# Optimization experiments

Measured on AMD Instinct MI355X. Metric: run time of the kernel, lower is better.

The kernel has to match this reference:

```python
import jax, jax.numpy as jnp
import numpy as np

B, S, T = 64, 48, 48
E, H = 512, 1024
V_SRC, V_TGT = 32000, 32000
PAD = 0


def setup_inputs() -> dict:
    key = jax.random.key(0)
    ks = jax.random.split(key, 24)
    def g(k, shape, scale=0.05):
        return jax.random.normal(k, shape, dtype=jnp.float32) * scale
    return {
        "src_ids": jax.random.randint(ks[0], (S, B), 0, V_SRC),
        "tgt_ids": jax.random.randint(ks[1], (T, B), 0, V_TGT),
        "src_lengths": S,
        "src_emb": g(ks[2], (V_SRC, E)).at[PAD].set(0.0),
        "tgt_emb": g(ks[3], (V_TGT, E)).at[PAD].set(0.0),
        "cnn_w": g(ks[4], (E, E, 2)),
        "cnn_b": g(ks[5], (E,)),
        "enc_Wih_f": g(ks[6], (4 * H, E)),
        "enc_Whh_f": g(ks[7], (4 * H, H)),
        "enc_bih_f": g(ks[8], (4 * H,)),
        "enc_bhh_f": g(ks[9], (4 * H,)),
        "enc_Wih_b": g(ks[10], (4 * H, E)),
        "enc_Whh_b": g(ks[11], (4 * H, H)),
        "enc_bih_b": g(ks[12], (4 * H,)),
        "enc_bhh_b": g(ks[13], (4 * H,)),
        "dec_Wih": g(ks[14], (4 * H, E + H)),
        "dec_Whh": g(ks[15], (4 * H, H)),
        "dec_bih": g(ks[16], (4 * H,)),
        "dec_bhh": g(ks[17], (4 * H,)),
        "Wh": g(ks[18], (H, 2 * H)),
        "Wc": g(ks[19], (H, 2 * H)),
        "Watt": g(ks[20], (H, 2 * H)),
        "Wcomb": g(ks[21], (H, 3 * H)),
        "Wvocab": g(ks[22], (V_TGT, H)),
    }


def _lstm_cell(x, h, c, Wih, Whh, bih, bhh):
    gates = x @ Wih.T + h @ Whh.T + bih + bhh  # (b, 4h)
    i, f, g, o = jnp.split(gates, 4, axis=-1)
    c_new = jax.nn.sigmoid(f) * c + jax.nn.sigmoid(i) * jnp.tanh(g)
    h_new = jax.nn.sigmoid(o) * jnp.tanh(c_new)
    return h_new, c_new


def _forward(src_ids, tgt_ids,
             src_emb, tgt_emb, cnn_w, cnn_b,
             enc_Wih_f, enc_Whh_f, enc_bih_f, enc_bhh_f,
             enc_Wih_b, enc_Whh_b, enc_bih_b, enc_bhh_b,
             dec_Wih, dec_Whh, dec_bih, dec_bhh,
             Wh, Wc, Watt, Wcomb, Wvocab):
    b = src_ids.shape[1]
    h = Wh.shape[0]
    # ---- encode ----
    X = src_emb[src_ids]                       # (S, b, E)
    Xc = jnp.transpose(X, (1, 2, 0))           # (b, E, S)
    # Conv1d kernel_size=2, padding='same' in torch pads (left=0, right=1)
    Xc = jax.lax.conv_general_dilated(Xc, cnn_w, window_strides=(1,),
                                      padding=[(0, 1)],
                                      dimension_numbers=("NCH", "OIH", "NCH"))
    Xc = Xc + cnn_b[None, :, None]
    X = jnp.transpose(Xc, (2, 0, 1))           # (S, b, E)

    h0 = jnp.zeros((b, h), dtype=X.dtype)
    def fstep(carry, x_t):
        hh, cc = carry
        hh, cc = _lstm_cell(x_t, hh, cc, enc_Wih_f, enc_Whh_f, enc_bih_f, enc_bhh_f)
        return (hh, cc), hh
    def bstep(carry, x_t):
        hh, cc = carry
        hh, cc = _lstm_cell(x_t, hh, cc, enc_Wih_b, enc_Whh_b, enc_bih_b, enc_bhh_b)
        return (hh, cc), hh
    (hf, cf), out_f = jax.lax.scan(fstep, (h0, h0), X)
    (hb, cb), out_b = jax.lax.scan(bstep, (h0, h0), X[::-1])
    out_b = out_b[::-1]
    enc_hiddens = jnp.concatenate([out_f, out_b], axis=-1)   # (S, b, 2h)
    enc_hiddens = jnp.transpose(enc_hiddens, (1, 0, 2))      # (b, S, 2h)
    dec_h = jnp.concatenate([hf, hb], axis=1) @ Wh.T         # (b, h)
    dec_c = jnp.concatenate([cf, cb], axis=1) @ Wc.T         # (b, h)

    # ---- decode ----
    enc_proj = enc_hiddens @ Watt.T            # (b, S, h)
    enc_mask = jnp.zeros((b, enc_hiddens.shape[1]), dtype=bool)  # all full length
    Y = tgt_emb[tgt_ids[:-1]]                  # (T-1, b, E)

    def dstep(carry, Y_t):
        hh, cc, o_prev = carry
        ybar = jnp.concatenate([o_prev, Y_t], axis=1)        # (b, h+E)
        hh, cc = _lstm_cell(ybar, hh, cc, dec_Wih, dec_Whh, dec_bih, dec_bhh)
        e_t = jnp.einsum("bh,bsh->bs", hh, enc_proj)
        e_t = jnp.where(enc_mask, -jnp.inf, e_t)
        alpha = jax.nn.softmax(e_t, axis=-1)
        a_t = jnp.einsum("bs,bsd->bd", alpha, enc_hiddens)   # (b, 2h)
        O_t = jnp.tanh(jnp.concatenate([a_t, hh], axis=1) @ Wcomb.T)  # dropout rate 0
        return (hh, cc, O_t), O_t

    o0 = jnp.zeros((b, h), dtype=X.dtype)
    _, combined = jax.lax.scan(dstep, (dec_h, dec_c, o0), Y)  # (T-1, b, h)

    P = jax.nn.log_softmax(combined @ Wvocab.T, axis=-1)      # (T-1, b, V)
    gold = tgt_ids[1:]                                        # (T-1, b)
    logp = jnp.take_along_axis(P, gold[..., None], axis=-1)[..., 0]
    tmask = (gold != PAD).astype(P.dtype)
    return (logp * tmask).sum(axis=0)                         # (b,)


def reference(src_ids, tgt_ids, src_lengths,
              src_emb, tgt_emb, cnn_w, cnn_b,
              enc_Wih_f, enc_Whh_f, enc_bih_f, enc_bhh_f,
              enc_Wih_b, enc_Whh_b, enc_bih_b, enc_bhh_b,
              dec_Wih, dec_Whh, dec_bih, dec_bhh,
              Wh, Wc, Watt, Wcomb, Wvocab):
    # src_lengths == S for every sentence (packed seq degenerates to full-length LSTM)
    return _forward(src_ids, tgt_ids, src_emb, tgt_emb, cnn_w, cnn_b,
                    enc_Wih_f, enc_Whh_f, enc_bih_f, enc_bhh_f,
                    enc_Wih_b, enc_Whh_b, enc_bih_b, enc_bhh_b,
                    dec_Wih, dec_Whh, dec_bih, dec_bhh,
                    Wh, Wc, Watt, Wcomb, Wvocab)
```

## Files before the change

kernel.cpp:

```cpp
#include <hip/hip_runtime.h>
#include <hip/hip_bf16.h>
#include <math.h>

using f32x4 = __attribute__((ext_vector_type(4))) float;
using s16x8 = __attribute__((ext_vector_type(8))) short;
typedef unsigned short u16;
typedef unsigned int u32;
typedef unsigned long long u64;

#define MFMA16(a,b,c) __builtin_amdgcn_mfma_f32_16x16x32_bf16(a,b,c,0,0,0)
#define SCOPE_A __HIP_MEMORY_SCOPE_AGENT
#define FP 16

__device__ __forceinline__ float bf2f(u16 u){
  union { u32 i; float f; } v; v.i = ((u32)u) << 16; return v.f;
}
__device__ __forceinline__ u16 f2bf(float f){
  union { float f; u32 i; } v; v.f = f;
  u32 x = v.i;
  return (u16)((x + 0x7fffu + ((x >> 16) & 1u)) >> 16);
}
__device__ __forceinline__ float sigm(float x){ return 1.0f/(1.0f + expf(-x)); }

__device__ __forceinline__ s16x8 pack8(const float* p){
  s16x8 r;
  #pragma unroll
  for (int i = 0; i < 8; ++i) r[i] = (short)f2bf(p[i]);
  return r;
}

__device__ __forceinline__ s16x8 coh_ld16B(const u16* p){
  union { u64 q[2]; s16x8 v; } u;
  u.q[0] = __hip_atomic_load((const u64*)p,       __ATOMIC_RELAXED, SCOPE_A);
  u.q[1] = __hip_atomic_load((const u64*)(p + 4), __ATOMIC_RELAXED, SCOPE_A);
  return u.v;
}
__device__ __forceinline__ u32 coh_ld32(const void* p){
  return __hip_atomic_load((const u32*)p, __ATOMIC_RELAXED, SCOPE_A);
}
__device__ __forceinline__ void coh_st32(void* p, u32 v){
  __hip_atomic_store((u32*)p, v, __ATOMIC_RELAXED, SCOPE_A);
}
__device__ __forceinline__ float u2f(u32 u){ union { u32 i; float f; } v; v.i = u; return v.f; }
__device__ __forceinline__ u32 f2u(float f){ union { float f; u32 i; } v; v.f = f; return v.i; }

__device__ __forceinline__ void poll(const int* flags, int n, int gen){
  for (int i = threadIdx.x; i < n; i += 256)
    while (__hip_atomic_load(flags + i*FP, __ATOMIC_RELAXED, SCOPE_A) < gen)
      __builtin_amdgcn_s_sleep(1);
  __syncthreads();
}
__device__ __forceinline__ void setflag(int* flag, int gen){
  __syncthreads();
  if (threadIdx.x == 0)
    __hip_atomic_store(flag, gen, __ATOMIC_RELAXED, SCOPE_A);
}

__device__ __forceinline__ void gemm_k1024_coh(
    const u16* ap, const char* wb0, const char* wb1, int xo, int addb,
    f32x4& a0, f32x4& a1)
{
  #pragma unroll
  for (int c = 0; c < 2; ++c){
    s16x8 st[16];
    #pragma unroll
    for (int q = 0; q < 16; ++q) st[q] = coh_ld16B(ap + c*512 + q*32);
    #pragma unroll
    for (int q = 0; q < 16; ++q){
      int cb = (addb + (c*512 + q*32)*2) ^ xo;
      a0 = MFMA16(st[q], *(const s16x8*)(wb0 + cb), a0);
      a1 = MFMA16(st[q], *(const s16x8*)(wb1 + cb), a1);
    }
  }
}

__global__ void k_zero(float* __restrict__ p, long n){
  long i = (long)blockIdx.x*blockDim.x + threadIdx.x;
  long st = (long)gridDim.x*blockDim.x;
  for (; i < n; i += st) p[i] = 0.0f;
}

__global__ void k_cast_bf16(const float* __restrict__ src, u16* __restrict__ dst, long n){
  long i = ((long)blockIdx.x*blockDim.x + threadIdx.x)*4;
  long st = (long)gridDim.x*blockDim.x*4;
  for (; i < n; i += st){
    float4 v = *(const float4*)(src + i);
    *(ushort4*)(dst + i) = make_ushort4(f2bf(v.x), f2bf(v.y), f2bf(v.z), f2bf(v.w));
  }
}

__global__ void k_addv(const float* __restrict__ a, const float* __restrict__ b,
                       float* __restrict__ d, int n){
  int i = blockIdx.x*blockDim.x + threadIdx.x;
  if (i < n) d[i] = a[i] + b[i];
}

__global__ void k_repack_conv(const float* __restrict__ w, u16* __restrict__ dst){
  int i = blockIdx.x*256 + threadIdx.x;
  int o = i >> 9, ii = i & 511;
  dst[(size_t)o*1024 + ii]       = f2bf(w[((size_t)o*512 + ii)*2 + 0]);
  dst[(size_t)o*1024 + 512 + ii] = f2bf(w[((size_t)o*512 + ii)*2 + 1]);
}

__global__ void k_build_wy(const float* __restrict__ dWih, u16* __restrict__ Wy){
  int i = blockIdx.x*256 + threadIdx.x;
  int r = i >> 9, c = i & 511;
  Wy[(size_t)r*512 + c] = f2bf(dWih[(size_t)r*1536 + 1024 + c]);
}

__global__ void k_split_wcomb(const float* __restrict__ Wcomb,
                              u16* __restrict__ Wca, u16* __restrict__ Whp){
  int r = blockIdx.x;
  for (int c = threadIdx.x; c < 2048; c += 256)
    Wca[(size_t)r*2048 + c] = f2bf(Wcomb[(size_t)r*3072 + c]);
  for (int c = threadIdx.x; c < 1024; c += 256)
    Whp[(size_t)r*1024 + c] = f2bf(Wcomb[(size_t)r*3072 + 2048 + c]);
}

__global__ void k_gather_src(const int* __restrict__ ids, const float* __restrict__ emb,
                             u16* __restrict__ Aconv){
  int s = blockIdx.x;
  int b = blockIdx.y;
  int e = threadIdx.x*4;
  float4 v = make_float4(0.f,0.f,0.f,0.f);
  if (s < 48){ int id = ids[s*64 + b]; v = *(const float4*)(emb + (size_t)id*512 + e); }
  ushort4 u = make_ushort4(f2bf(v.x), f2bf(v.y), f2bf(v.z), f2bf(v.w));
  if (s < 48) *(ushort4*)(Aconv + ((size_t)(s*64 + b))*1024 + e) = u;
  if (s >= 1) *(ushort4*)(Aconv + ((size_t)((s-1)*64 + b))*1024 + 512 + e) = u;
}

__global__ void k_gather_y(const int* __restrict__ ids, const float* __restrict__ emb,
                           u16* __restrict__ Y){
  int t = blockIdx.x; int b = blockIdx.y; int e = threadIdx.x*4;
  int id = ids[t*64 + b];
  float4 v = *(const float4*)(emb + (size_t)id*512 + e);
  *(ushort4*)(Y + ((size_t)(t*64 + b))*512 + e) = make_ushort4(f2bf(v.x), f2bf(v.y), f2bf(v.z), f2bf(v.w));
}

template<bool OUT_BF16>
__global__ __launch_bounds__(256) void k_gemm(
    const u16* __restrict__ A0, long lda0,
    const u16* __restrict__ A1, long lda1, int ksplit,
    const u16* __restrict__ W, int K,
    void* __restrict__ Out, long ldc,
    const float* __restrict__ bias)
{
  __shared__ __align__(16) u16 As[64][72];
  __shared__ __align__(16) u16 Ws[64][72];
  const int t = threadIdx.x;
  const int m0 = blockIdx.x*64, n0 = blockIdx.y*64;
  const int w = t >> 6, l = t & 63, lr = l & 15, lh = l >> 4;
  const int sr = t >> 2, sk = (t & 3) << 4;

  f32x4 acc[4] = {{0,0,0,0},{0,0,0,0},{0,0,0,0},{0,0,0,0}};

  for (int kc = 0; kc < K; kc += 64){
    {
      const u16* wp = W + (size_t)(n0 + sr)*K + kc + sk;
      *(s16x8*)&Ws[sr][sk]     = *(const s16x8*)wp;
      *(s16x8*)&Ws[sr][sk + 8] = *(const s16x8*)(wp + 8);
    }
    {
      const u16* ap = (kc < ksplit)
        ? A0 + (size_t)(m0 + sr)*lda0 + kc
        : A1 + (size_t)(m0 + sr)*lda1 + (kc - ksplit);
      ap += sk;
      *(s16x8*)&As[sr][sk]     = *(const s16x8*)ap;
      *(s16x8*)&As[sr][sk + 8] = *(const s16x8*)(ap + 8);
    }
    __syncthreads();
    #pragma unroll
    for (int kk = 0; kk < 64; kk += 32){
      s16x8 a = *(const s16x8*)&As[w*16 + lr][kk + lh*8];
      #pragma unroll
      for (int ct = 0; ct < 4; ++ct){
        s16x8 bfr = *(const s16x8*)&Ws[ct*16 + lr][kk + lh*8];
        acc[ct] = MFMA16(a, bfr, acc[ct]);
      }
    }
    __syncthreads();
  }
  #pragma unroll
  for (int ct = 0; ct < 4; ++ct){
    #pragma unroll
    for (int rr = 0; rr < 4; ++rr){
      long row = m0 + w*16 + lh*4 + rr;
      long col = n0 + ct*16 + lr;
      float v = acc[ct][rr];
      if (bias) v += bias[col];
      long oi = row*ldc + col;
      if (OUT_BF16) ((u16*)Out)[oi] = f2bf(v);
      else          ((float*)Out)[oi] = v;
    }
  }
}

__global__ __launch_bounds__(256) void k_enc_persist(
    const float* __restrict__ WhhF, const float* __restrict__ WhhB,
    const u16* __restrict__ Gf, const u16* __restrict__ Gb,
    u16* __restrict__ hF0, u16* __restrict__ hF1,
    u16* __restrict__ hB0, u16* __restrict__ hB1,
    float* __restrict__ cF, float* __restrict__ cB,
    u16* __restrict__ Aatt, u16* __restrict__ cfbf, u16* __restrict__ cbbf,
    int* Eflags)
{
  extern __shared__ char smem[];
  const int t = threadIdx.x, blk = blockIdx.x;
  const int dir = blk >> 6;
  const int j0 = (blk & 63) << 4;
  const float* Wsrc = dir ? WhhB : WhhF;
  const u16* G = dir ? Gb : Gf;
  float* c = dir ? cB : cF;
  u16* cobf = dir ? cbbf : cfbf;
  u16* h0 = dir ? hB0 : hF0;
  u16* h1 = dir ? hB1 : hF1;

  for (int q = t; q < 64*128; q += 256){
    int row = q >> 7;
    int ck = (q & 127) << 3;
    int wrow = ((row >> 4)*1024) + j0 + (row & 15);
    s16x8 pk = pack8(Wsrc + (size_t)wrow*1024 + ck);
    *(s16x8*)(smem + row*2048 + ((ck*2) ^ ((row & 7) << 4))) = pk;
  }
  __syncthreads();

  const int w = t >> 6, l = t & 63, lr = l & 15, lh = l >> 4;
  const int lane_m = w*16 + lr;
  const int koff = lh*8;
  const char* wp0 = smem + lr*2048;
  const char* wp1 = smem + (16 + lr)*2048;
  const char* wp2 = smem + (32 + lr)*2048;
  const char* wp3 = smem + (48 + lr)*2048;
  const int xo = (lr & 7) << 4;
  const int j = j0 + lr;
  int* myflags = Eflags + dir*64*FP;
  const int myidx = blk & 63;

  for (int s = 0; s < 48; ++s){
    const u16* hin = (s & 1) ? h1 : h0;
    u16* hout      = (s & 1) ? h0 : h1;
    const int time = dir ? 47 - s : s;
    if (s) poll(myflags, 64, s);
    f32x4 a0 = {0,0,0,0}, a1 = {0,0,0,0}, a2 = {0,0,0,0}, a3 = {0,0,0,0};
    const u16* ap = hin + (size_t)lane_m*1024 + koff;
    #pragma unroll
    for (int cc = 0; cc < 2; ++cc){
      s16x8 st[16];
      #pragma unroll
      for (int q = 0; q < 16; ++q) st[q] = coh_ld16B(ap + cc*512 + q*32);
      #pragma unroll
      for (int q = 0; q < 16; ++q){
        int cb = ((cc*512 + q*32 + koff)*2) ^ xo;
        a0 = MFMA16(st[q], *(const s16x8*)(wp0 + cb), a0);
        a1 = MFMA16(st[q], *(const s16x8*)(wp1 + cb), a1);
        a2 = MFMA16(st[q], *(const s16x8*)(wp2 + cb), a2);
        a3 = MFMA16(st[q], *(const s16x8*)(wp3 + cb), a3);
      }
    }
    #pragma unroll
    for (int rr = 0; rr < 4; ++rr){
      int b = w*16 + lh*4 + rr;
      size_t grow = ((size_t)time*64 + b)*4096;
      float gi = a0[rr] + bf2f(G[grow + j]);
      float gf = a1[rr] + bf2f(G[grow + 1024 + j]);
      float gg = a2[rr] + bf2f(G[grow + 2048 + j]);
      float go = a3[rr] + bf2f(G[grow + 3072 + j]);
      float cn = sigm(gf)*c[b*1024 + j] + sigm(gi)*tanhf(gg);
      float hn = sigm(go)*tanhf(cn);
      c[b*1024 + j] = cn;
      u16 hb = f2bf(hn);
      u32 hi2 = __shfl_down((u32)hb, 1);
      if ((lr & 1) == 0)
        coh_st32((u32*)hout + ((b*1024 + j) >> 1), (u32)hb | (hi2 << 16));
      Aatt[((size_t)b*48 + time)*2048 + dir*1024 + j] = hb;
      if (s == 47) cobf[b*1024 + j] = f2bf(cn);
    }
    setflag(myflags + myidx*FP, s + 1);
  }
}

__global__ __launch_bounds__(256) void k_dec_persist(
    const float* __restrict__ dWih, const float* __restrict__ dWhh,
    const u16* __restrict__ Gy,
    const u16* __restrict__ encP, const u16* __restrict__ encWc,
    const u16* __restrict__ Whp,
    u16* __restrict__ hbf0, u16* __restrict__ hbf1,
    float* __restrict__ cdec,
    float* __restrict__ hpart, u16* __restrict__ Cbf,
    const u16* __restrict__ obf_zero,
    int* Gflags, int* G2flags, int* Cflags)
{
  extern __shared__ char smem[];
  const int t = threadIdx.x, blk = blockIdx.x;
  const int w = t >> 6, l = t & 63, lr = l & 15, lh = l >> 4;
  const int lane_m = w*16 + lr;
  const int koff = lh*8;
  const int xo = (lr & 7) << 4;

  if (blk < 128){
    const int j0 = blk << 3;
    for (int q = t; q < 32*256; q += 256){
      int row = q >> 8;
      int ck = (q & 255) << 3;
      int wrow = ((row >> 3)*1024) + j0 + (row & 7);
      const float* src = (ck < 1024) ? dWih + (size_t)wrow*1536 + ck
                                     : dWhh + (size_t)wrow*1024 + (ck - 1024);
      s16x8 pk = pack8(src);
      *(s16x8*)(smem + row*4096 + ((ck*2) ^ ((row & 7) << 4))) = pk;
    }
    char* WhpL = smem + 131072;
    for (int q = t; q < 8*128; q += 256){
      int row = q >> 7, ck = (q & 127) << 3;
      s16x8 v = *(const s16x8*)(Whp + (size_t)(j0 + row)*1024 + ck);
      *(s16x8*)(WhpL + row*2048 + ((ck*2) ^ ((row & 7) << 4))) = v;
    }
    __syncthreads();
    const char* wp0 = smem + lr*4096;
    const char* wp1 = smem + (16 + lr)*4096;
    const char* wph = WhpL + (lr & 7)*2048;
    const int jj = lr & 7, gsel = lr >> 3;
    const int j = j0 + jj;

    s16x8 hreg[32];
    {
      const u16* ap = hbf0 + (size_t)lane_m*1024 + koff;
      #pragma unroll
      for (int q = 0; q < 32; ++q) hreg[q] = coh_ld16B(ap + q*32);
    }

    for (int tt = 0; tt < 47; ++tt){
      u16* hout = (tt & 1) ? hbf0 : hbf1;
      f32x4 a0 = {0,0,0,0}, a1 = {0,0,0,0};
      #pragma unroll
      for (int q = 0; q < 32; ++q){
        int cb = ((1024 + q*32 + koff)*2) ^ xo;
        a0 = MFMA16(hreg[q], *(const s16x8*)(wp0 + cb), a0);
        a1 = MFMA16(hreg[q], *(const s16x8*)(wp1 + cb), a1);
      }
      if (tt) poll(Cflags, 64, tt);
      const u16* Ao = tt ? (Cbf + (size_t)(tt - 1)*65536) : obf_zero;
      gemm_k1024_coh(Ao + (size_t)lane_m*1024 + koff, wp0, wp1, xo, koff*2, a0, a1);
      #pragma unroll
      for (int rr = 0; rr < 4; ++rr){
        float v0 = a0[rr], v1 = a1[rr];
        float p0 = __shfl_xor(v0, 8, 64);
        float p1 = __shfl_xor(v1, 8, 64);
        if (gsel == 0){
          int b = w*16 + lh*4 + rr;
          size_t grow = ((size_t)tt*64 + b)*4096;
          float gi = v0 + bf2f(Gy[grow + j]);
          float gf = p0 + bf2f(Gy[grow + 1024 + j]);
          float gg = v1 + bf2f(Gy[grow + 2048 + j]);
          float go = p1 + bf2f(Gy[grow + 3072 + j]);
          float cn = sigm(gf)*cdec[b*1024 + j] + sigm(gi)*tanhf(gg);
          float hn = sigm(go)*tanhf(cn);
          cdec[b*1024 + j] = cn;
          u16 hb = f2bf(hn);
          u32 hi2 = __shfl_down((u32)hb, 1);
          if ((jj & 1) == 0)
            coh_st32((u32*)hout + ((b*1024 + j) >> 1), (u32)hb | (hi2 << 16));
        }
      }
      setflag(Gflags + blk*FP, tt + 1);
      poll(Gflags, 128, tt + 1);
      {
        const u16* ap = hout + (size_t)lane_m*1024 + koff;
        #pragma unroll
        for (int q = 0; q < 32; ++q) hreg[q] = coh_ld16B(ap + q*32);
      }
      f32x4 hp = {0,0,0,0};
      #pragma unroll
      for (int q = 0; q < 32; ++q){
        int cb = ((q*32 + koff)*2) ^ xo;
        s16x8 bw = {0,0,0,0,0,0,0,0};
        if (lr < 8) bw = *(const s16x8*)(wph + cb);
        hp = MFMA16(hreg[q], bw, hp);
      }
      if (lr < 8){
        #pragma unroll
        for (int rr = 0; rr < 4; ++rr)
          coh_st32(&hpart[(size_t)(w*16 + lh*4 + rr)*1024 + j0 + lr], f2u(hp[rr]));
      }
      setflag(G2flags + blk*FP, tt + 1);
    }
  } else {
    const int b = blk - 128;
    u16* encPL = (u16*)smem;
    float* hs  = (float*)(smem + 98304);
    float* es  = (float*)(smem + 102400);
    float* al  = es + 48;
    float* sred= al + 48;
    for (int q = t; q < 48*128; q += 256){
      int row = q >> 7, ck = (q & 127) << 3;
      *(s16x8*)&encPL[row*1024 + ck] =
        *(const s16x8*)(encP + ((size_t)b*48 + row)*1024 + ck);
    }
    __syncthreads();

    for (int tt = 0; tt < 47; ++tt){
      poll(Gflags, 128, tt + 1);
      const u16* hpost = (tt & 1) ? hbf0 : hbf1;
      const u32* h32 = (const u32*)hpost + b*512;
      for (int i = t; i < 512; i += 256){
        u32 v = coh_ld32(h32 + i);
        hs[2*i]     = bf2f((u16)(v & 0xffff));
        hs[2*i + 1] = bf2f((u16)(v >> 16));
      }
      __syncthreads();
      for (int s2 = w; s2 < 48; s2 += 4){
        float p = 0.f;
        #pragma unroll
        for (int i = 0; i < 16; ++i)
          p += hs[l + 64*i]*bf2f(encPL[s2*1024 + l + 64*i]);
        #pragma unroll
        for (int d = 32; d >= 1; d >>= 1) p += __shfl_xor(p, d, 64);
        if (l == 0) es[s2] = p;
      }
      __syncthreads();
      if (t == 0){
        float m = es[0];
        for (int s2 = 1; s2 < 48; ++s2) m = fmaxf(m, es[s2]);
        float su = 0.f;
        for (int s2 = 0; s2 < 48; ++s2) su += expf(es[s2] - m);
        sred[0] = m; sred[1] = 1.0f/su;
      }
      __syncthreads();
      if (t < 48) al[t] = expf(es[t] - sred[0])*sred[1];
      __syncthreads();
      poll(G2flags, 128, tt + 1);
      int c0 = t*4;
      float4 hpv;
      {
        union { u64 q[2]; float4 v; } u;
        const u64* hp64 = (const u64*)(hpart + (size_t)b*1024 + c0);
        u.q[0] = __hip_atomic_load(hp64,     __ATOMIC_RELAXED, SCOPE_A);
        u.q[1] = __hip_atomic_load(hp64 + 1, __ATOMIC_RELAXED, SCOPE_A);
        hpv = u.v;
      }
      float acc0 = 0.f, acc1 = 0.f, acc2 = 0.f, acc3 = 0.f;
      const u16* ew = encWc + (size_t)b*48*1024 + c0;
      #pragma unroll 4
      for (int s2 = 0; s2 < 48; ++s2){
        float wgt = al[s2];
        ushort4 e4 = *(const ushort4*)(ew + (size_t)s2*1024);
        acc0 += wgt*bf2f(e4.x); acc1 += wgt*bf2f(e4.y);
        acc2 += wgt*bf2f(e4.z); acc3 += wgt*bf2f(e4.w);
      }
      float v0 = tanhf(hpv.x + acc0), v1 = tanhf(hpv.y + acc1);
      float v2 = tanhf(hpv.z + acc2), v3 = tanhf(hpv.w + acc3);
      size_t oi = (size_t)tt*65536 + (size_t)b*1024 + c0;
      coh_st32((u32*)Cbf + (oi >> 1),     (u32)f2bf(v0) | ((u32)f2bf(v1) << 16));
      coh_st32((u32*)Cbf + (oi >> 1) + 1, (u32)f2bf(v2) | ((u32)f2bf(v3) << 16));
      setflag(Cflags + b*FP, tt + 1);
    }
  }
}

#define VNS 25
__global__ __launch_bounds__(256) void k_vocab_lse(
    const u16* __restrict__ Cbf, const u16* __restrict__ Wv, float2* __restrict__ partials)
{
  __shared__ __align__(16) u16 As[128][72];
  __shared__ __align__(16) u16 Bs[128][72];
  __shared__ float2 mg[128][2];
  int rb = blockIdx.x, sp = blockIdx.y;
  int m0 = rb*128;
  int t = threadIdx.x, w = t >> 6, l = t & 63, lr = l & 15, lh = l >> 4;
  int wr = w >> 1, wc = w & 1;
  int sr = t >> 1, sk = (t & 1) << 5;

  float mrun[4][4], srun[4][4];
  #pragma unroll
  for (int m = 0; m < 4; ++m)
    #pragma unroll
    for (int rr = 0; rr < 4; ++rr){ mrun[m][rr] = -INFINITY; srun[m][rr] = 0.f; }

  for (int nt = 0; nt < 10; ++nt){
    int n0 = sp*1280 + nt*128;
    f32x4 acc[4][4];
    #pragma unroll
    for (int m = 0; m < 4; ++m)
      #pragma unroll
      for (int n = 0; n < 4; ++n) acc[m][n] = (f32x4){0,0,0,0};

    for (int kc = 0; kc < 1024; kc += 64){
      int ar = m0 + sr; if (ar > 3007) ar = 3007;
      const u16* ap = Cbf + (size_t)ar*1024 + kc + sk;
      const u16* wp = Wv + (size_t)(n0 + sr)*1024 + kc + sk;
      #pragma unroll
      for (int q = 0; q < 4; ++q){
        *(s16x8*)&As[sr][sk + q*8] = *(const s16x8*)(ap + q*8);
        *(s16x8*)&Bs[sr][sk + q*8] = *(const s16x8*)(wp + q*8);
      }
      __syncthreads();
      #pragma unroll
      for (int kk = 0; kk < 64; kk += 32){
        s16x8 af[4], bf[4];
        #pragma unroll
        for (int m = 0; m < 4; ++m)
          af[m] = *(const s16x8*)&As[wr*64 + m*16 + lr][kk + lh*8];
        #pragma unroll
        for (int n = 0; n < 4; ++n)
          bf[n] = *(const s16x8*)&Bs[wc*64 + n*16 + lr][kk + lh*8];
        #pragma unroll
        for (int m = 0; m < 4; ++m)
          #pragma unroll
          for (int n = 0; n < 4; ++n)
            acc[m][n] = MFMA16(af[m], bf[n], acc[m][n]);
      }
      __syncthreads();
    }
    #pragma unroll
    for (int m = 0; m < 4; ++m){
      #pragma unroll
      for (int rr = 0; rr < 4; ++rr){
        float tm = fmaxf(fmaxf(acc[m][0][rr], acc[m][1][rr]),
                         fmaxf(acc[m][2][rr], acc[m][3][rr]));
        #pragma unroll
        for (int d = 1; d < 16; d <<= 1) tm = fmaxf(tm, __shfl_xor(tm, d, 64));
        float ts = expf(acc[m][0][rr] - tm) + expf(acc[m][1][rr] - tm)
                 + expf(acc[m][2][rr] - tm) + expf(acc[m][3][rr] - tm);
        #pragma unroll
        for (int d = 1; d < 16; d <<= 1) ts += __shfl_xor(ts, d, 64);
        if (tm > mrun[m][rr]){ srun[m][rr] = srun[m][rr]*expf(mrun[m][rr] - tm) + ts; mrun[m][rr] = tm; }
        else srun[m][rr] += ts*expf(tm - mrun[m][rr]);
      }
    }
  }
  __syncthreads();
  if (lr == 0){
    #pragma unroll
    for (int m = 0; m < 4; ++m)
      #pragma unroll
      for (int rr = 0; rr < 4; ++rr)
        mg[wr*64 + m*16 + lh*4 + rr][wc] = make_float2(mrun[m][rr], srun[m][rr]);
  }
  __syncthreads();
  if (t < 128){
    float2 p0 = mg[t][0], p1 = mg[t][1];
    float m = fmaxf(p0.x, p1.x);
    float s = p0.y*expf(p0.x - m) + p1.y*expf(p1.x - m);
    long row = m0 + t;
    if (row < 3008) partials[row*VNS + sp] = make_float2(m, s);
  }
}

__global__ void k_lse(const float2* __restrict__ partials, float* __restrict__ lse){
  int r = blockIdx.x*256 + threadIdx.x;
  if (r >= 3008) return;
  float m = -INFINITY, s = 0.f;
  for (int i = 0; i < VNS; ++i){
    float2 p = partials[r*VNS + i];
    if (p.x > m){ s = s*expf(m - p.x) + p.y; m = p.x; }
    else s += p.y*expf(p.x - m);
  }
  lse[r] = m + logf(s);
}

__global__ __launch_bounds__(256) void k_gold(const u16* __restrict__ Cbf,
                                              const u16* __restrict__ Wv,
                                              const int* __restrict__ tgt,
                                              float* __restrict__ gold){
  int w = threadIdx.x >> 6, l = threadIdx.x & 63;
  int r = blockIdx.x*4 + w;
  int tt = r >> 6, b = r & 63;
  int gid = tgt[(tt + 1)*64 + b];
  const u16* cp = Cbf + (size_t)r*1024;
  const u16* wp = Wv + (size_t)gid*1024;
  float p = 0.f;
  for (int i = l; i < 1024; i += 64) p += bf2f(cp[i])*bf2f(wp[i]);
  for (int d = 32; d >= 1; d >>= 1) p += __shfl_xor(p, d, 64);
  if (l == 0) gold[r] = p;
}

__global__ void k_final(const float* __restrict__ gold, const float* __restrict__ lse,
                        const int* __restrict__ tgt, float* __restrict__ out){
  int b = threadIdx.x;
  if (b >= 64) return;
  float acc = 0.f;
  for (int t = 0; t < 47; ++t){
    int gid = tgt[(t + 1)*64 + b];
    if (gid != 0) acc += gold[t*64 + b] - lse[t*64 + b];
  }
  out[b] = acc;
}

extern "C" void kernel_launch(void* const* d_in, const int* in_sizes, int n_in,
                              void* d_out, int out_size, void* d_ws, size_t ws_size,
                              hipStream_t stream)
{
  (void)in_sizes; (void)n_in; (void)out_size; (void)ws_size;
  const int*   src_ids = (const int*)d_in[0];
  const int*   tgt_ids = (const int*)d_in[1];
  const float* src_emb = (const float*)d_in[3];
  const float* tgt_emb = (const float*)d_in[4];
  const float* cnn_w   = (const float*)d_in[5];
  const float* cnn_b   = (const float*)d_in[6];
  const float* eWih_f  = (const float*)d_in[7];
  const float* eWhh_f  = (const float*)d_in[8];
  const float* ebih_f  = (const float*)d_in[9];
  const float* ebhh_f  = (const float*)d_in[10];
  const float* eWih_b  = (const float*)d_in[11];
  const float* eWhh_b  = (const float*)d_in[12];
  const float* ebih_b  = (const float*)d_in[13];
  const float* ebhh_b  = (const float*)d_in[14];
  const float* dWih    = (const float*)d_in[15];
  const float* dWhh    = (const float*)d_in[16];
  const float* dbih    = (const float*)d_in[17];
  const float* dbhh    = (const float*)d_in[18];
  const float* Wh      = (const float*)d_in[19];
  const float* Wc      = (const float*)d_in[20];
  const float* Watt    = (const float*)d_in[21];
  const float* Wcomb   = (const float*)d_in[22];
  const float* Wvocab  = (const float*)d_in[23];

  char* ws = (char*)d_ws;
  size_t off = 0;
  auto alloc = [&](size_t bytes)->char*{
    char* p = ws + off;
    off = (off + bytes + 255) & ~(size_t)255;
    return p;
  };

  u16* hF0      = (u16*)alloc((size_t)65536*2);
  u16* hB0      = (u16*)alloc((size_t)65536*2);
  float* cF     = (float*)alloc((size_t)65536*4);
  float* cB     = (float*)alloc((size_t)65536*4);
  u16* obf_zero = (u16*)alloc((size_t)65536*2);
  int* bar      = (int*)alloc(40960);
  size_t zero_floats = ((size_t)131072*3 + (size_t)262144*2 + 40960)/4;
  int* Eflags  = bar;
  int* Gflags  = bar + 2048;
  int* G2flags = bar + 4096;
  int* Cflags  = bar + 6144;

  u16* hF1      = (u16*)alloc((size_t)65536*2);
  u16* hB1      = (u16*)alloc((size_t)65536*2);

  u16* Wconv_bf = (u16*)alloc((size_t)512*1024*2);
  u16* Wih_f_bf = (u16*)alloc((size_t)4096*512*2);
  u16* Wih_b_bf = (u16*)alloc((size_t)4096*512*2);
  u16* Wy_bf    = (u16*)alloc((size_t)4096*512*2);
  u16* Wh_bf    = (u16*)alloc((size_t)1024*2048*2);
  u16* Wc_bf    = (u16*)alloc((size_t)1024*2048*2);
  u16* Watt_bf  = (u16*)alloc((size_t)1024*2048*2);
  u16* Wca_bf   = (u16*)alloc((size_t)1024*2048*2);
  u16* Whp_bf   = (u16*)alloc((size_t)1024*1024*2);
  u16* Wv_bf    = (u16*)alloc((size_t)32000*1024*2);
  float* benc_f = (float*)alloc(4096*4);
  float* benc_b = (float*)alloc(4096*4);
  float* bdec   = (float*)alloc(4096*4);

  u16* Aconv    = (u16*)alloc((size_t)3072*1024*2);
  u16* Xc       = (u16*)alloc((size_t)3072*512*2);
  u16* Gf       = (u16*)alloc((size_t)3072*4096*2);
  u16* Gb       = (u16*)alloc((size_t)3072*4096*2);
  u16* Ybf      = (u16*)alloc((size_t)3008*512*2);
  u16* Gy       = (u16*)alloc((size_t)3008*4096*2);
  u16* Aatt     = (u16*)alloc((size_t)3072*2048*2);
  u16* encP     = (u16*)alloc((size_t)3072*1024*2);
  u16* encWc    = (u16*)alloc((size_t)3072*1024*2);
  u16* cfbf     = (u16*)alloc((size_t)65536*2);
  u16* cbbf     = (u16*)alloc((size_t)65536*2);
  u16* hbf0     = (u16*)alloc((size_t)65536*2);
  u16* hbf1     = (u16*)alloc((size_t)65536*2);
  float* cdec   = (float*)alloc((size_t)65536*4);
  float* hpartD = (float*)alloc((size_t)65536*4);
  u16* Cbf      = (u16*)alloc((size_t)3008*1024*2);
  float2* partials=(float2*)alloc((size_t)3008*VNS*8);
  float* lse    = (float*)alloc(3008*4);
  float* gold   = (float*)alloc(3008*4);

  k_zero<<<256, 256, 0, stream>>>((float*)hF0, (long)zero_floats);

  auto cgrid = [](long n)->int{ long g = (n/4 + 255)/256; return (int)(g > 1024 ? 1024 : g); };
  k_cast_bf16<<<cgrid(4096*512), 256, 0, stream>>>(eWih_f, Wih_f_bf, (long)4096*512);
  k_cast_bf16<<<cgrid(4096*512), 256, 0, stream>>>(eWih_b, Wih_b_bf, (long)4096*512);
  k_cast_bf16<<<cgrid(1024*2048), 256, 0, stream>>>(Wh, Wh_bf, (long)1024*2048);
  k_cast_bf16<<<cgrid(1024*2048), 256, 0, stream>>>(Wc, Wc_bf, (long)1024*2048);
  k_cast_bf16<<<cgrid(1024*2048), 256, 0, stream>>>(Watt, Watt_bf, (long)1024*2048);
  k_cast_bf16<<<cgrid((long)32000*1024), 256, 0, stream>>>(Wvocab, Wv_bf, (long)32000*1024);

  k_addv<<<16, 256, 0, stream>>>(ebih_f, ebhh_f, benc_f, 4096);
  k_addv<<<16, 256, 0, stream>>>(ebih_b, ebhh_b, benc_b, 4096);
  k_addv<<<16, 256, 0, stream>>>(dbih, dbhh, bdec, 4096);

  k_repack_conv<<<1024, 256, 0, stream>>>(cnn_w, Wconv_bf);
  k_build_wy<<<8192, 256, 0, stream>>>(dWih, Wy_bf);
  k_split_wcomb<<<1024, 256, 0, stream>>>(Wcomb, Wca_bf, Whp_bf);

  k_gather_src<<<dim3(49, 64), 128, 0, stream>>>(src_ids, src_emb, Aconv);
  k_gather_y<<<dim3(47, 64), 128, 0, stream>>>(tgt_ids, tgt_emb, Ybf);

  k_gemm<true><<<dim3(48, 8), 256, 0, stream>>>(
      Aconv, 1024, Aconv, 1024, 1024, Wconv_bf, 1024, Xc, 512, cnn_b);
  k_gemm<true><<<dim3(48, 64), 256, 0, stream>>>(
      Xc, 512, Xc, 512, 512, Wih_f_bf, 512, Gf, 4096, benc_f);
  k_gemm<true><<<dim3(48, 64), 256, 0, stream>>>(
      Xc, 512, Xc, 512, 512, Wih_b_bf, 512, Gb, 4096, benc_b);
  k_gemm<true><<<dim3(47, 64), 256, 0, stream>>>(
      Ybf, 512, Ybf, 512, 512, Wy_bf, 512, Gy, 4096, bdec);

  k_enc_persist<<<128, 256, 131072, stream>>>(
      eWhh_f, eWhh_b, Gf, Gb, hF0, hF1, hB0, hB1, cF, cB,
      Aatt, cfbf, cbbf, Eflags);

  k_gemm<true><<<dim3(1, 16), 256, 0, stream>>>(
      hF0, 1024, hB0, 1024, 1024, Wh_bf, 2048, hbf0, 1024, nullptr);
  k_gemm<false><<<dim3(1, 16), 256, 0, stream>>>(
      cfbf, 1024, cbbf, 1024, 1024, Wc_bf, 2048, cdec, 1024, nullptr);
  k_gemm<true><<<dim3(48, 16), 256, 0, stream>>>(
      Aatt, 2048, Aatt, 2048, 2048, Watt_bf, 2048, encP, 1024, nullptr);
  k_gemm<true><<<dim3(48, 16), 256, 0, stream>>>(
      Aatt, 2048, Aatt, 2048, 2048, Wca_bf, 2048, encWc, 1024, nullptr);

  k_dec_persist<<<192, 256, 147456, stream>>>(
      dWih, dWhh, Gy, encP, encWc, Whp_bf, hbf0, hbf1, cdec,
      hpartD, Cbf, obf_zero, Gflags, G2flags, Cflags);

  k_vocab_lse<<<dim3(24, VNS), 256, 0, stream>>>(Cbf, Wv_bf, partials);
  k_lse<<<12, 256, 0, stream>>>(partials, lse);
  k_gold<<<752, 256, 0, stream>>>(Cbf, Wv_bf, tgt_ids, gold);
  k_final<<<1, 64, 0, stream>>>(gold, lse, tgt_ids, (float*)d_out);
}
```

Before: 2.769 ms.

## Use per-step hidden buffers with plain loads and repack gate precompute layout

Replaces the ping-pong hidden-state buffers in the encoder and decoder persistent kernels with one buffer per timestep. Because no address is ever rewritten, the agent-scope atomic loads can become plain vector loads without stale-cache hazards. The input-gate GEMMs now write a packed [time][j][gate][batch] layout, so each lane's four gate reads are close together instead of 1024 elements apart. This costs more memory and leaves cross-block visibility depending on never-before-touched addresses and relaxed flag ordering, which is a correctness risk.

Result: faster. 2.585 ms (-6.6%).

```diff
diff --git a/kernel.cpp b/kernel.cpp
--- a/kernel.cpp
+++ b/kernel.cpp
@@ -29,15 +29,6 @@
   return r;
 }
 
-__device__ __forceinline__ s16x8 coh_ld16B(const u16* p){
-  union { u64 q[2]; s16x8 v; } u;
-  u.q[0] = __hip_atomic_load((const u64*)p,       __ATOMIC_RELAXED, SCOPE_A);
-  u.q[1] = __hip_atomic_load((const u64*)(p + 4), __ATOMIC_RELAXED, SCOPE_A);
-  return u.v;
-}
-__device__ __forceinline__ u32 coh_ld32(const void* p){
-  return __hip_atomic_load((const u32*)p, __ATOMIC_RELAXED, SCOPE_A);
-}
 __device__ __forceinline__ void coh_st32(void* p, u32 v){
   __hip_atomic_store((u32*)p, v, __ATOMIC_RELAXED, SCOPE_A);
 }
@@ -56,7 +47,7 @@
     __hip_atomic_store(flag, gen, __ATOMIC_RELAXED, SCOPE_A);
 }
 
-__device__ __forceinline__ void gemm_k1024_coh(
+__device__ __forceinline__ void gemm_k1024(
     const u16* ap, const char* wb0, const char* wb1, int xo, int addb,
     f32x4& a0, f32x4& a1)
 {
@@ -64,7 +55,7 @@
   for (int c = 0; c < 2; ++c){
     s16x8 st[16];
     #pragma unroll
-    for (int q = 0; q < 16; ++q) st[q] = coh_ld16B(ap + c*512 + q*32);
+    for (int q = 0; q < 16; ++q) st[q] = *(const s16x8*)(ap + c*512 + q*32);
     #pragma unroll
     for (int q = 0; q < 16; ++q){
       int cb = (addb + (c*512 + q*32)*2) ^ xo;
@@ -137,7 +128,7 @@
   *(ushort4*)(Y + ((size_t)(t*64 + b))*512 + e) = make_ushort4(f2bf(v.x), f2bf(v.y), f2bf(v.z), f2bf(v.w));
 }
 
-template<bool OUT_BF16>
+template<bool OUT_BF16, bool PACKG>
 __global__ __launch_bounds__(256) void k_gemm(
     const u16* __restrict__ A0, long lda0,
     const u16* __restrict__ A1, long lda1, int ksplit,
@@ -188,18 +179,23 @@
       long col = n0 + ct*16 + lr;
       float v = acc[ct][rr];
       if (bias) v += bias[col];
-      long oi = row*ldc + col;
-      if (OUT_BF16) ((u16*)Out)[oi] = f2bf(v);
-      else          ((float*)Out)[oi] = v;
+      if (PACKG){
+        long time = row >> 6, b = row & 63, g = col >> 10, j = col & 1023;
+        ((u16*)Out)[((time*1024 + j)*4 + g)*64 + b] = f2bf(v);
+      } else {
+        long oi = row*ldc + col;
+        if (OUT_BF16) ((u16*)Out)[oi] = f2bf(v);
+        else          ((float*)Out)[oi] = v;
+      }
     }
   }
 }
 
 __global__ __launch_bounds__(256) void k_enc_persist(
     const float* __restrict__ WhhF, const float* __restrict__ WhhB,
-    const u16* __restrict__ Gf, const u16* __restrict__ Gb,
-    u16* __restrict__ hF0, u16* __restrict__ hF1,
-    u16* __restrict__ hB0, u16* __restrict__ hB1,
+    const u16* __restrict__ GfP, const u16* __restrict__ GbP,
+    u16* __restrict__ hEF, u16* __restrict__ hEB,
+    const u16* __restrict__ hzero,
     float* __restrict__ cF, float* __restrict__ cB,
     u16* __restrict__ Aatt, u16* __restrict__ cfbf, u16* __restrict__ cbbf,
     int* Eflags)
@@ -209,11 +205,10 @@
   const int dir = blk >> 6;
   const int j0 = (blk & 63) << 4;
   const float* Wsrc = dir ? WhhB : WhhF;
-  const u16* G = dir ? Gb : Gf;
+  const u16* GP = dir ? GbP : GfP;
   float* c = dir ? cB : cF;
   u16* cobf = dir ? cbbf : cfbf;
-  u16* h0 = dir ? hB0 : hF0;
-  u16* h1 = dir ? hB1 : hF1;
+  u16* hE = dir ? hEB : hEF;
 
   for (int q = t; q < 64*128; q += 256){
     int row = q >> 7;
@@ -237,8 +232,8 @@
   const int myidx = blk & 63;
 
   for (int s = 0; s < 48; ++s){
-    const u16* hin = (s & 1) ? h1 : h0;
-    u16* hout      = (s & 1) ? h0 : h1;
+    const u16* hin = s ? (hE + (size_t)(s - 1)*65536) : hzero;
+    u16* hout      = hE + (size_t)s*65536;
     const int time = dir ? 47 - s : s;
     if (s) poll(myflags, 64, s);
     f32x4 a0 = {0,0,0,0}, a1 = {0,0,0,0}, a2 = {0,0,0,0}, a3 = {0,0,0,0};
@@ -247,7 +242,7 @@
     for (int cc = 0; cc < 2; ++cc){
       s16x8 st[16];
       #pragma unroll
-      for (int q = 0; q < 16; ++q) st[q] = coh_ld16B(ap + cc*512 + q*32);
+      for (int q = 0; q < 16; ++q) st[q] = *(const s16x8*)(ap + cc*512 + q*32);
       #pragma unroll
       for (int q = 0; q < 16; ++q){
         int cb = ((cc*512 + q*32 + koff)*2) ^ xo;
@@ -260,11 +255,11 @@
     #pragma unroll
     for (int rr = 0; rr < 4; ++rr){
       int b = w*16 + lh*4 + rr;
-      size_t grow = ((size_t)time*64 + b)*4096;
-      float gi = a0[rr] + bf2f(G[grow + j]);
-      float gf = a1[rr] + bf2f(G[grow + 1024 + j]);
-      float gg = a2[rr] + bf2f(G[grow + 2048 + j]);
-      float go = a3[rr] + bf2f(G[grow + 3072 + j]);
+      const u16* gp = GP + (((size_t)time*1024 + j)*4)*64 + b;
+      float gi = a0[rr] + bf2f(gp[0]);
+      float gf = a1[rr] + bf2f(gp[64]);
+      float gg = a2[rr] + bf2f(gp[128]);
+      float go = a3[rr] + bf2f(gp[192]);
       float cn = sigm(gf)*c[b*1024 + j] + sigm(gi)*tanhf(gg);
       float hn = sigm(go)*tanhf(cn);
       c[b*1024 + j] = cn;
@@ -281,12 +276,12 @@
 
 __global__ __launch_bounds__(256) void k_dec_persist(
     const float* __restrict__ dWih, const float* __restrict__ dWhh,
-    const u16* __restrict__ Gy,
+    const u16* __restrict__ GyP,
     const u16* __restrict__ encP, const u16* __restrict__ encWc,
     const u16* __restrict__ Whp,
-    u16* __restrict__ hbf0, u16* __restrict__ hbf1,
+    const u16* __restrict__ hbinit, u16* __restrict__ hD,
     float* __restrict__ cdec,
-    float* __restrict__ hpart, u16* __restrict__ Cbf,
+    float* __restrict__ hp, u16* __restrict__ Cbf,
     const u16* __restrict__ obf_zero,
     int* Gflags, int* G2flags, int* Cflags)
 {
@@ -323,13 +318,13 @@
 
     s16x8 hreg[32];
     {
-      const u16* ap = hbf0 + (size_t)lane_m*1024 + koff;
-      #pragma unroll
-      for (int q = 0; q < 32; ++q) hreg[q] = coh_ld16B(ap + q*32);
+      const u16* ap = hbinit + (size_t)lane_m*1024 + koff;
+      #pragma unroll
+      for (int q = 0; q < 32; ++q) hreg[q] = *(const s16x8*)(ap + q*32);
     }
 
     for (int tt = 0; tt < 47; ++tt){
-      u16* hout = (tt & 1) ? hbf0 : hbf1;
+      u16* hout = hD + (size_t)tt*65536;
       f32x4 a0 = {0,0,0,0}, a1 = {0,0,0,0};
       #pragma unroll
       for (int q = 0; q < 32; ++q){
@@ -339,7 +334,7 @@
       }
       if (tt) poll(Cflags, 64, tt);
       const u16* Ao = tt ? (Cbf + (size_t)(tt - 1)*65536) : obf_zero;
-      gemm_k1024_coh(Ao + (size_t)lane_m*1024 + koff, wp0, wp1, xo, koff*2, a0, a1);
+      gemm_k1024(Ao + (size_t)lane_m*1024 + koff, wp0, wp1, xo, koff*2, a0, a1);
       #pragma unroll
       for (int rr = 0; rr < 4; ++rr){
         float v0 = a0[rr], v1 = a1[rr];
@@ -347,11 +342,11 @@
         float p1 = __shfl_xor(v1, 8, 64);
         if (gsel == 0){
           int b = w*16 + lh*4 + rr;
-          size_t grow = ((size_t)tt*64 + b)*4096;
-          float gi = v0 + bf2f(Gy[grow + j]);
-          float gf = p0 + bf2f(Gy[grow + 1024 + j]);
-          float gg = v1 + bf2f(Gy[grow + 2048 + j]);
-          float go = p1 + bf2f(Gy[grow + 3072 + j]);
+          const u16* gp = GyP + (((size_t)tt*1024 + j)*4)*64 + b;
+          float gi = v0 + bf2f(gp[0]);
+          float gf = p0 + bf2f(gp[64]);
+          float gg = v1 + bf2f(gp[128]);
+          float go = p1 + bf2f(gp[192]);
           float cn = sigm(gf)*cdec[b*1024 + j] + sigm(gi)*tanhf(gg);
           float hn = sigm(go)*tanhf(cn);
           cdec[b*1024 + j] = cn;
@@ -366,20 +361,21 @@
       {
         const u16* ap = hout + (size_t)lane_m*1024 + koff;
         #pragma unroll
-        for (int q = 0; q < 32; ++q) hreg[q] = coh_ld16B(ap + q*32);
-      }
-      f32x4 hp = {0,0,0,0};
+        for (int q = 0; q < 32; ++q) hreg[q] = *(const s16x8*)(ap + q*32);
+      }
+      f32x4 hpacc = {0,0,0,0};
       #pragma unroll
       for (int q = 0; q < 32; ++q){
         int cb = ((q*32 + koff)*2) ^ xo;
         s16x8 bw = {0,0,0,0,0,0,0,0};
         if (lr < 8) bw = *(const s16x8*)(wph + cb);
-        hp = MFMA16(hreg[q], bw, hp);
+        hpacc = MFMA16(hreg[q], bw, hpacc);
       }
       if (lr < 8){
+        float* hpout = hp + (size_t)tt*65536;
         #pragma unroll
         for (int rr = 0; rr < 4; ++rr)
-          coh_st32(&hpart[(size_t)(w*16 + lh*4 + rr)*1024 + j0 + lr], f2u(hp[rr]));
+          coh_st32(&hpout[(size_t)(w*16 + lh*4 + rr)*1024 + j0 + lr], f2u(hpacc[rr]));
       }
       setflag(G2flags + blk*FP, tt + 1);
     }
@@ -399,12 +395,13 @@
 
     for (int tt = 0; tt < 47; ++tt){
       poll(Gflags, 128, tt + 1);
-      const u16* hpost = (tt & 1) ? hbf0 : hbf1;
-      const u32* h32 = (const u32*)hpost + b*512;
-      for (int i = t; i < 512; i += 256){
-        u32 v = coh_ld32(h32 + i);
-        hs[2*i]     = bf2f((u16)(v & 0xffff));
-        hs[2*i + 1] = bf2f((u16)(v >> 16));
+      const u16* hrow = hD + (size_t)tt*65536 + (size_t)b*1024;
+      {
+        ushort4 v4 = ((const ushort4*)hrow)[t];
+        hs[4*t]     = bf2f(v4.x);
+        hs[4*t + 1] = bf2f(v4.y);
+        hs[4*t + 2] = bf2f(v4.z);
+        hs[4*t + 3] = bf2f(v4.w);
       }
       __syncthreads();
       for (int s2 = w; s2 < 48; s2 += 4){
@@ -429,14 +426,7 @@
       __syncthreads();
       poll(G2flags, 128, tt + 1);
       int c0 = t*4;
-      float4 hpv;
-      {
-        union { u64 q[2]; float4 v; } u;
-        const u64* hp64 = (const u64*)(hpart + (size_t)b*1024 + c0);
-        u.q[0] = __hip_atomic_load(hp64,     __ATOMIC_RELAXED, SCOPE_A);
-        u.q[1] = __hip_atomic_load(hp64 + 1, __ATOMIC_RELAXED, SCOPE_A);
-        hpv = u.v;
-      }
+      float4 hpv = *(const float4*)(hp + (size_t)tt*65536 + (size_t)b*1024 + c0);
       float acc0 = 0.f, acc1 = 0.f, acc2 = 0.f, acc3 = 0.f;
       const u16* ew = encWc + (size_t)b*48*1024 + c0;
       #pragma unroll 4
@@ -622,20 +612,15 @@
     return p;
   };
 
-  u16* hF0      = (u16*)alloc((size_t)65536*2);
-  u16* hB0      = (u16*)alloc((size_t)65536*2);
   float* cF     = (float*)alloc((size_t)65536*4);
   float* cB     = (float*)alloc((size_t)65536*4);
   u16* obf_zero = (u16*)alloc((size_t)65536*2);
   int* bar      = (int*)alloc(40960);
-  size_t zero_floats = ((size_t)131072*3 + (size_t)262144*2 + 40960)/4;
+  size_t zero_floats = ((size_t)262144*2 + 131072 + 40960)/4;
   int* Eflags  = bar;
   int* Gflags  = bar + 2048;
   int* G2flags = bar + 4096;
   int* Cflags  = bar + 6144;
-
-  u16* hF1      = (u16*)alloc((size_t)65536*2);
-  u16* hB1      = (u16*)alloc((size_t)65536*2);
 
   u16* Wconv_bf = (u16*)alloc((size_t)512*1024*2);
   u16* Wih_f_bf = (u16*)alloc((size_t)4096*512*2);
@@ -653,25 +638,27 @@
 
   u16* Aconv    = (u16*)alloc((size_t)3072*1024*2);
   u16* Xc       = (u16*)alloc((size_t)3072*512*2);
-  u16* Gf       = (u16*)alloc((size_t)3072*4096*2);
-  u16* Gb       = (u16*)alloc((size_t)3072*4096*2);
+  u16* GfP      = (u16*)alloc((size_t)48*1024*256*2);
+  u16* GbP      = (u16*)alloc((size_t)48*1024*256*2);
+  u16* GyP      = (u16*)alloc((size_t)47*1024*256*2);
   u16* Ybf      = (u16*)alloc((size_t)3008*512*2);
-  u16* Gy       = (u16*)alloc((size_t)3008*4096*2);
   u16* Aatt     = (u16*)alloc((size_t)3072*2048*2);
   u16* encP     = (u16*)alloc((size_t)3072*1024*2);
   u16* encWc    = (u16*)alloc((size_t)3072*1024*2);
+  u16* hEF      = (u16*)alloc((size_t)48*65536*2);
+  u16* hEB      = (u16*)alloc((size_t)48*65536*2);
   u16* cfbf     = (u16*)alloc((size_t)65536*2);
   u16* cbbf     = (u16*)alloc((size_t)65536*2);
-  u16* hbf0     = (u16*)alloc((size_t)65536*2);
-  u16* hbf1     = (u16*)alloc((size_t)65536*2);
+  u16* hbinit   = (u16*)alloc((size_t)65536*2);
+  u16* hD       = (u16*)alloc((size_t)47*65536*2);
   float* cdec   = (float*)alloc((size_t)65536*4);
-  float* hpartD = (float*)alloc((size_t)65536*4);
+  float* hp     = (float*)alloc((size_t)47*65536*4);
   u16* Cbf      = (u16*)alloc((size_t)3008*1024*2);
   float2* partials=(float2*)alloc((size_t)3008*VNS*8);
   float* lse    = (float*)alloc(3008*4);
   float* gold   = (float*)alloc(3008*4);
 
-  k_zero<<<256, 256, 0, stream>>>((float*)hF0, (long)zero_floats);
+  k_zero<<<256, 256, 0, stream>>>(cF, (long)zero_floats);
 
   auto cgrid = [](long n)->int{ long g = (n/4 + 255)/256; return (int)(g > 1024 ? 1024 : g); };
   k_cast_bf16<<<cgrid(4096*512), 256, 0, stream>>>(eWih_f, Wih_f_bf, (long)4096*512);
@@ -692,31 +679,32 @@
   k_gather_src<<<dim3(49, 64), 128, 0, stream>>>(src_ids, src_emb, Aconv);
   k_gather_y<<<dim3(47, 64), 128, 0, stream>>>(tgt_ids, tgt_emb, Ybf);
 
-  k_gemm<true><<<dim3(48, 8), 256, 0, stream>>>(
+  k_gemm<true, false><<<dim3(48, 8), 256, 0, stream>>>(
       Aconv, 1024, Aconv, 1024, 1024, Wconv_bf, 1024, Xc, 512, cnn_b);
-  k_gemm<true><<<dim3(48, 64), 256, 0, stream>>>(
-      Xc, 512, Xc, 512, 512, Wih_f_bf, 512, Gf, 4096, benc_f);
-  k_gemm<true><<<dim3(48, 64), 256, 0, stream>>>(
-      Xc, 512, Xc, 512, 512, Wih_b_bf, 512, Gb, 4096, benc_b);
-  k_gemm<true><<<dim3(47, 64), 256, 0, stream>>>(
-      Ybf, 512, Ybf, 512, 512, Wy_bf, 512, Gy, 4096, bdec);
+  k_gemm<true, true><<<dim3(48, 64), 256, 0, stream>>>(
+      Xc, 512, Xc, 512, 512, Wih_f_bf, 512, GfP, 0, benc_f);
+  k_gemm<true, true><<<dim3(48, 64), 256, 0, stream>>>(
+      Xc, 512, Xc, 512, 512, Wih_b_bf, 512, GbP, 0, benc_b);
+  k_gemm<true, true><<<dim3(47, 64), 256, 0, stream>>>(
+      Ybf, 512, Ybf, 512, 512, Wy_bf, 512, GyP, 0, bdec);
 
   k_enc_persist<<<128, 256, 131072, stream>>>(
-      eWhh_f, eWhh_b, Gf, Gb, hF0, hF1, hB0, hB1, cF, cB,
+      eWhh_f, eWhh_b, GfP, GbP, hEF, hEB, obf_zero, cF, cB,
       Aatt, cfbf, cbbf, Eflags);
 
-  k_gemm<true><<<dim3(1, 16), 256, 0, stream>>>(
-      hF0, 1024, hB0, 1024, 1024, Wh_bf, 2048, hbf0, 1024, nullptr);
-  k_gemm<false><<<dim3(1, 16), 256, 0, stream>>>(
+  k_gemm<true, false><<<dim3(1, 16), 256, 0, stream>>>(
+      hEF + (size_t)47*65536, 1024, hEB + (size_t)47*65536, 1024, 1024,
+      Wh_bf, 2048, hbinit, 1024, nullptr);
+  k_gemm<false, false><<<dim3(1, 16), 256, 0, stream>>>(
       cfbf, 1024, cbbf, 1024, 1024, Wc_bf, 2048, cdec, 1024, nullptr);
-  k_gemm<true><<<dim3(48, 16), 256, 0, stream>>>(
+  k_gemm<true, false><<<dim3(48, 16), 256, 0, stream>>>(
       Aatt, 2048, Aatt, 2048, 2048, Watt_bf, 2048, encP, 1024, nullptr);
-  k_gemm<true><<<dim3(48, 16), 256, 0, stream>>>(
+  k_gemm<true, false><<<dim3(48, 16), 256, 0, stream>>>(
       Aatt, 2048, Aatt, 2048, 2048, Wca_bf, 2048, encWc, 1024, nullptr);
 
   k_dec_persist<<<192, 256, 147456, stream>>>(
-      dWih, dWhh, Gy, encP, encWc, Whp_bf, hbf0, hbf1, cdec,
-      hpartD, Cbf, obf_zero, Gflags, G2flags, Cflags);
+      dWih, dWhh, GyP, encP, encWc, Whp_bf, hbinit, hD, cdec,
+      hp, Cbf, obf_zero, Gflags, G2flags, Cflags);
 
   k_vocab_lse<<<dim3(24, VNS), 256, 0, stream>>>(Cbf, Wv_bf, partials);
   k_lse<<<12, 256, 0, stream>>>(partials, lse);
```
